# Performance work log

Measured on AMD Instinct MI355X. Metric: run time of the kernel, lower is better.

The kernel has to match this reference:

```python
import jax, jax.numpy as jnp
import numpy as np

T_SCHEDULE = 999.0
LOG_2PI = float(np.log(2.0 * np.pi))


def setup_inputs() -> dict:
    key = jax.random.key(0)
    k1, k2, k3 = jax.random.split(key, 3)
    xt = jax.random.normal(k1, (128, 3, 32, 32), dtype=jnp.float32)
    # integer-style diffusion timesteps in [0, 900); divided by t_schedule=999 inside
    t = jax.random.uniform(k2, (128,), dtype=jnp.float32) * 900.0
    gt_images = jax.random.normal(k3, (20000, 3, 32, 32), dtype=jnp.float32)
    return {"xt": xt, "t": t, "gt_images": gt_images}


def reference(xt, t, gt_images):
    # AnalyticFlow.forward_fast
    B = xt.shape[0]
    N = gt_images.shape[0]
    x = jax.lax.stop_gradient(xt.reshape(B, -1))  # original detaches x
    gt = gt_images.reshape(N, -1)                 # [N, D]
    D = x.shape[-1]
    tt = t / T_SCHEDULE                           # [B]
    sig = 1.0 - tt                                # [B]
    # log N(term_2; 0, I) summed over D, where term_2 = (x - t*gt)/(1-t).
    # ||x - t*gt||^2 = ||x||^2 - 2 t x.gt + t^2 ||gt||^2  (avoids B*N*D tensor)
    x2 = jnp.sum(x * x, axis=-1)                  # [B]
    g2 = jnp.sum(gt * gt, axis=-1)                # [N]
    xg = x @ gt.T                                 # [B, N] GEMM
    sq = x2[:, None] - 2.0 * tt[:, None] * xg + (tt * tt)[:, None] * g2[None, :]
    log_p = -0.5 * sq / (sig * sig)[:, None] - 0.5 * D * LOG_2PI  # [B, N]
    log_p = log_p - jnp.max(log_p)                # global-max shift as in original
    eta = jax.nn.softmax(log_p, axis=1)           # [B, N], rows sum to 1
    # drift = mean_n (N*eta_n) * (gt_n - x)/(1-t) = (eta @ gt - x)/(1-t)
    drift = (eta @ gt - x) / sig[:, None]         # [B, D]
    return drift.reshape(xt.shape)
```

## Files before the change

kernel.cpp:

```cpp
#include <hip/hip_runtime.h>
#include <hip/hip_bf16.h>
#include <stdint.h>

#define B_SZ   128
#define D_SZ   3072
#define N_SZ   20000
#define NPAD   20480
#define BN     (B_SZ * NPAD)
#define BD     (B_SZ * D_SZ)
#define KC_S   4
#define KC_D   20

typedef __attribute__((ext_vector_type(8))) short          short8;
typedef __attribute__((ext_vector_type(4))) float          f32x4;
typedef __attribute__((ext_vector_type(4))) unsigned short u16x4;
typedef __attribute__((ext_vector_type(2))) unsigned int   uint2v;

__device__ __forceinline__ unsigned short f2bf(float f) {
    unsigned u = __float_as_uint(f);
    u += 0x7FFFu + ((u >> 16) & 1u);
    return (unsigned short)(u >> 16);
}
__device__ __forceinline__ float bf2f(unsigned short h) {
    return __uint_as_float(((unsigned)h) << 16);
}
__device__ __forceinline__ unsigned fkey_enc(float f) {
    unsigned b = __float_as_uint(f);
    return (b & 0x80000000u) ? ~b : (b | 0x80000000u);
}
__device__ __forceinline__ float fkey_dec(unsigned u) {
    return __uint_as_float((u & 0x80000000u) ? (u ^ 0x80000000u) : ~u);
}

__device__ __forceinline__ void gl_lds16(const void* g, void* l) {
    __builtin_amdgcn_global_load_lds(
        (const __attribute__((address_space(1))) void*)g,
        (__attribute__((address_space(3))) void*)l, 16, 0, 0);
}

__device__ __forceinline__ int swz(int r, int q) { return q ^ ((r >> 1) & 3); }

__global__ __launch_bounds__(256) void zero_small(float* __restrict__ p)
{
    p[blockIdx.x * 256 + threadIdx.x] = 0.f;
}

__global__ __launch_bounds__(256) void prep_x(const float* __restrict__ x,
                                              unsigned short* __restrict__ xhi,
                                              unsigned short* __restrict__ xlo)
{
    int i = blockIdx.x * 256 + threadIdx.x;
    float v = x[i];
    unsigned short h = f2bf(v);
    xhi[i] = h;
    xlo[i] = f2bf(v - bf2f(h));
}

__global__ __launch_bounds__(256) void scores_kernel(
        const float* __restrict__ gt,
        const unsigned short* __restrict__ xhi,
        const unsigned short* __restrict__ xlo,
        float* __restrict__ XG_part,
        float* __restrict__ G2,
        unsigned short* __restrict__ Gh)
{
    __shared__ __align__(16) unsigned short Xhi_t[128 * 32];
    __shared__ __align__(16) unsigned short Xlo_t[128 * 32];
    __shared__ __align__(16) unsigned short Ghi_t[64 * 32];
    __shared__ __align__(16) unsigned short Glo_t[64 * 32];

    const int tid   = threadIdx.x;
    const int kc    = blockIdx.x & 3;
    const int nt    = blockIdx.x >> 2;
    const int nbase = nt * 64;
    const int kcb   = kc * 768;

    const int lane = tid & 63;
    const int wave = tid >> 6;
    const int mh = wave & 1;
    const int nh = wave >> 1;
    const int lm = lane & 15;
    const int qd = lane >> 4;

    const int gn = tid >> 2;
    const int gq = tid & 3;
    const int ng0 = nbase + gn;
    int grow = ng0 > N_SZ - 1 ? N_SZ - 1 : ng0;
    const float* gp0 = gt + (size_t)grow * D_SZ + kcb + gq * 8;
    unsigned short* ghp0 = Gh + (size_t)ng0 * D_SZ + kcb + gq * 8;
    const int gwr = gn * 32 + swz(gn, gq) * 8;

    int xsrc[2], xdst[2];
    #pragma unroll
    for (int i = 0; i < 2; i++) {
        int o = (i * 256 + tid) * 16;
        int r = o >> 6;
        int j = (o >> 4) & 3;
        xdst[i] = o;
        xsrc[i] = r * D_SZ + kcb + swz(r, j) * 8;
    }

    float g2acc = 0.0f;

    f32x4 acc[4][2];
    #pragma unroll
    for (int i = 0; i < 4; i++)
        #pragma unroll
        for (int j = 0; j < 2; j++)
            acc[i][j] = (f32x4){0.f, 0.f, 0.f, 0.f};

    for (int k0 = 0; k0 < 768; k0 += 32) {
        #pragma unroll
        for (int i = 0; i < 2; i++) {
            gl_lds16(xhi + xsrc[i] + k0, (char*)Xhi_t + xdst[i]);
            gl_lds16(xlo + xsrc[i] + k0, (char*)Xlo_t + xdst[i]);
        }
        f32x4 v0 = *(const f32x4*)(gp0 + k0);
        f32x4 v1 = *(const f32x4*)(gp0 + k0 + 4);
        short8 h8, l8;
        #pragma unroll
        for (int j = 0; j < 4; j++) {
            float a = v0[j], b = v1[j];
            unsigned short ha = f2bf(a), hb = f2bf(b);
            h8[j]     = (short)ha;  h8[j + 4] = (short)hb;
            l8[j]     = (short)f2bf(a - bf2f(ha));
            l8[j + 4] = (short)f2bf(b - bf2f(hb));
            g2acc += a * a + b * b;
        }
        *(short8*)&Ghi_t[gwr] = h8;
        *(short8*)&Glo_t[gwr] = l8;
        if (ng0 < N_SZ) *(short8*)(ghp0 + k0) = h8;

        __syncthreads();

        short8 bhi[2], blo[2];
        #pragma unroll
        for (int ni = 0; ni < 2; ni++) {
            int r = nh * 32 + ni * 16 + lm;
            int sl = r * 32 + swz(r, qd) * 8;
            bhi[ni] = *(short8*)&Ghi_t[sl];
            blo[ni] = *(short8*)&Glo_t[sl];
        }
        #pragma unroll
        for (int mi = 0; mi < 4; mi++) {
            int r = mh * 64 + mi * 16 + lm;
            int sl = r * 32 + swz(r, qd) * 8;
            short8 ahi = *(short8*)&Xhi_t[sl];
            short8 alo = *(short8*)&Xlo_t[sl];
            #pragma unroll
            for (int ni = 0; ni < 2; ni++) {
                acc[mi][ni] = __builtin_amdgcn_mfma_f32_16x16x32_bf16(ahi, bhi[ni], acc[mi][ni], 0, 0, 0);
                acc[mi][ni] = __builtin_amdgcn_mfma_f32_16x16x32_bf16(ahi, blo[ni], acc[mi][ni], 0, 0, 0);
                acc[mi][ni] = __builtin_amdgcn_mfma_f32_16x16x32_bf16(alo, bhi[ni], acc[mi][ni], 0, 0, 0);
            }
        }
        __syncthreads();
    }

    g2acc += __shfl_xor(g2acc, 1);
    g2acc += __shfl_xor(g2acc, 2);
    if (gq == 0 && ng0 < N_SZ) atomicAdd(&G2[ng0], g2acc);

    float* XGp = XG_part + (size_t)kc * BN;
    #pragma unroll
    for (int mi = 0; mi < 4; mi++) {
        #pragma unroll
        for (int ni = 0; ni < 2; ni++) {
            int ncol = nh * 32 + ni * 16 + lm;
            int ng = nbase + ncol;
            if (ng < N_SZ) {
                #pragma unroll
                for (int i = 0; i < 4; i++) {
                    int m = mh * 64 + mi * 16 + qd * 4 + i;
                    XGp[(size_t)m * NPAD + ng] = acc[mi][ni][i];
                }
            }
        }
    }
}

__global__ __launch_bounds__(256) void sum4max(
        const float* __restrict__ XG_part, const float* __restrict__ G2,
        const float* __restrict__ tarr, float* __restrict__ XG,
        unsigned* __restrict__ Mkey)
{
    const int tid = threadIdx.x;
    const int b = blockIdx.x / 20;
    const int i = (blockIdx.x * 256 + tid) * 4;
    __shared__ float wred[4];

    f32x4 s = (f32x4){0.f, 0.f, 0.f, 0.f};
    #pragma unroll
    for (int kc = 0; kc < KC_S; kc++)
        s += *(const f32x4*)(XG_part + (size_t)kc * BN + i);
    *(f32x4*)(XG + i) = s;

    float tt  = tarr[b] / 999.0f;
    float sig = 1.0f - tt;
    float inv = 1.0f / (sig * sig);
    float c1 = tt * inv, c2 = 0.5f * tt * tt * inv;
    int n = i - b * NPAD;

    float mx = -3.402823466e+38f;
    #pragma unroll
    for (int j = 0; j < 4; j++)
        if (n + j < N_SZ) mx = fmaxf(mx, c1 * s[j] - c2 * G2[n + j]);
    #pragma unroll
    for (int o = 32; o > 0; o >>= 1) mx = fmaxf(mx, __shfl_xor(mx, o));
    if ((tid & 63) == 0) wred[tid >> 6] = mx;
    __syncthreads();
    if (tid == 0) {
        mx = fmaxf(fmaxf(wred[0], wred[1]), fmaxf(wred[2], wred[3]));
        atomicMax(&Mkey[b], fkey_enc(mx));
    }
}

__global__ __launch_bounds__(256) void expk(
        const float* __restrict__ XG, const float* __restrict__ G2,
        const float* __restrict__ tarr, const unsigned* __restrict__ Mkey,
        unsigned short* __restrict__ P, float* __restrict__ L)
{
    const int b  = blockIdx.x >> 3;
    const int ch = blockIdx.x & 7;
    const int tid = threadIdx.x;
    float tt  = tarr[b] / 999.0f;
    float sig = 1.0f - tt;
    float inv = 1.0f / (sig * sig);
    float c1 = tt * inv, c2 = 0.5f * tt * tt * inv;
    float m = fkey_dec(Mkey[b]);
    const float* xg = XG + (size_t)b * NPAD;
    unsigned short* prow = P + (size_t)b * NPAD;
    __shared__ float wred[4];

    float sum = 0.f;
    int n0 = ch * 2560;
    for (int n = n0 + tid; n < n0 + 2560; n += 256) {
        float p = 0.f;
        if (n < N_SZ) { p = expf(c1 * xg[n] - c2 * G2[n] - m); sum += p; }
        prow[n] = f2bf(p);
    }
    #pragma unroll
    for (int o = 32; o > 0; o >>= 1) sum += __shfl_xor(sum, o);
    if ((tid & 63) == 0) wred[tid >> 6] = sum;
    __syncthreads();
    if (tid == 0) atomicAdd(&L[b], wred[0] + wred[1] + wred[2] + wred[3]);
}

__global__ __launch_bounds__(256) void drift_kernel(
        const unsigned short* __restrict__ Gh,
        const unsigned short* __restrict__ P,
        float* __restrict__ Dacc_part)
{
    __shared__ __align__(16) unsigned short Pt[128 * 32];
    __shared__ __align__(16) unsigned short Gt[128 * 40];

    const int tid = threadIdx.x;
    const int nt = blockIdx.x % 24;
    const int kc = blockIdx.x / 24;
    const int dbase = nt * 128;

    const int lane = tid & 63;
    const int wave = tid >> 6;
    const int mh = wave & 1;
    const int dh = wave >> 1;
    const int lm = lane & 15;
    const int qd = lane >> 4;

    const int dg = tid & 31;
    const int kq = tid >> 5;

    int psrc[2], pdst[2];
    #pragma unroll
    for (int i = 0; i < 2; i++) {
        int o = (i * 256 + tid) * 16;
        int r = o >> 6;
        int j = (o >> 4) & 3;
        pdst[i] = o;
        psrc[i] = r * NPAD + kc * 1024 + swz(r, j) * 8;
    }

    f32x4 acc[4][4];
    #pragma unroll
    for (int i = 0; i < 4; i++)
        #pragma unroll
        for (int j = 0; j < 4; j++)
            acc[i][j] = (f32x4){0.f, 0.f, 0.f, 0.f};

    for (int s = 0; s < 32; s++) {
        int kb = kc * 1024 + s * 32;
        #pragma unroll
        for (int i = 0; i < 2; i++)
            gl_lds16(P + psrc[i] + s * 32, (char*)Pt + pdst[i]);
        u16x4 row[4];
        #pragma unroll
        for (int i = 0; i < 4; i++) {
            int kg = kb + kq * 4 + i;
            if (kg > N_SZ - 1) kg = N_SZ - 1;
            row[i] = *(const u16x4*)(Gh + (size_t)kg * D_SZ + dbase + dg * 4);
        }
        #pragma unroll
        for (int j = 0; j < 4; j++) {
            unsigned u01 = (unsigned)row[0][j] | ((unsigned)row[1][j] << 16);
            unsigned u23 = (unsigned)row[2][j] | ((unsigned)row[3][j] << 16);
            uint2v pk = (uint2v){u01, u23};
            __builtin_memcpy((char*)Gt + (size_t)(dg * 4 + j) * 80 + kq * 8, &pk, 8);
        }
        __syncthreads();

        short8 af[4], bf8[4];
        #pragma unroll
        for (int mi = 0; mi < 4; mi++) {
            int r = mh * 64 + mi * 16 + lm;
            af[mi] = *(short8*)&Pt[r * 32 + swz(r, qd) * 8];
        }
        #pragma unroll
        for (int ni = 0; ni < 4; ni++)
            bf8[ni] = *(short8*)((char*)Gt + (size_t)(dh * 64 + ni * 16 + lm) * 80 + qd * 16);
        #pragma unroll
        for (int mi = 0; mi < 4; mi++)
            #pragma unroll
            for (int ni = 0; ni < 4; ni++)
                acc[mi][ni] = __builtin_amdgcn_mfma_f32_16x16x32_bf16(af[mi], bf8[ni], acc[mi][ni], 0, 0, 0);
        __syncthreads();
    }

    float* Dp = Dacc_part + (size_t)kc * BD;
    #pragma unroll
    for (int mi = 0; mi < 4; mi++)
        #pragma unroll
        for (int ni = 0; ni < 4; ni++) {
            int d = dbase + dh * 64 + ni * 16 + lm;
            #pragma unroll
            for (int i = 0; i < 4; i++) {
                int m = mh * 64 + mi * 16 + qd * 4 + i;
                Dp[(size_t)m * D_SZ + d] = acc[mi][ni][i];
            }
        }
}

__global__ __launch_bounds__(256) void epilogue_kernel(
        const float* __restrict__ Dacc_part, const float* __restrict__ L,
        const float* __restrict__ x, const float* __restrict__ tarr,
        float* __restrict__ out)
{
    int i = (blockIdx.x * 256 + threadIdx.x) * 4;
    int b = i / D_SZ;
    f32x4 s = (f32x4){0.f, 0.f, 0.f, 0.f};
    #pragma unroll
    for (int kc = 0; kc < KC_D; kc++)
        s += *(const f32x4*)(Dacc_part + (size_t)kc * BD + i);
    float tt = tarr[b] / 999.0f;
    float sig = 1.0f - tt;
    float invL = 1.0f / L[b];
    f32x4 xv = *(const f32x4*)(x + i);
    f32x4 o;
    #pragma unroll
    for (int j = 0; j < 4; j++) o[j] = (s[j] * invL - xv[j]) / sig;
    *(f32x4*)(out + i) = o;
}

extern "C" void kernel_launch(void* const* d_in, const int* in_sizes, int n_in,
                              void* d_out, int out_size, void* d_ws, size_t ws_size,
                              hipStream_t stream)
{
    const float* xt = (const float*)d_in[0];
    const float* t  = (const float*)d_in[1];
    const float* gt = (const float*)d_in[2];
    float* out = (float*)d_out;

    char* ws = (char*)d_ws;
    float*          XG_part  = (float*)(ws + 0);
    float*          XG       = (float*)(ws + 41943040);
    float*          Dacc_part= (float*)(ws + 52428800);
    float*          G2       = (float*)(ws + 83886080);
    unsigned*       Mkey     = (unsigned*)(ws + 83968000);
    float*          L        = (float*)(ws + 83968512);
    unsigned short* Xhi      = (unsigned short*)(ws + 83969024);
    unsigned short* Xlo      = (unsigned short*)(ws + 84755456);
    unsigned short* P        = (unsigned short*)(ws + 85541888);
    unsigned short* Gh       = (unsigned short*)(ws + 90784768);

    zero_small    <<<   81, 256, 0, stream>>>(G2);
    prep_x        <<< 1536, 256, 0, stream>>>(xt, Xhi, Xlo);
    scores_kernel <<< 1252, 256, 0, stream>>>(gt, Xhi, Xlo, XG_part, G2, Gh);
    sum4max       <<< 2560, 256, 0, stream>>>(XG_part, G2, t, XG, Mkey);
    expk          <<< 1024, 256, 0, stream>>>(XG, G2, t, Mkey, P, L);
    drift_kernel  <<<  480, 256, 0, stream>>>(Gh, P, Dacc_part);
    epilogue_kernel<<< 384, 256, 0, stream>>>(Dacc_part, L, xt, t, out);
}
```

Before: 498.3 us.

## Double-buffer LDS in scores and drift GEMMs and double drift K-split

Both GEMM kernels now use two LDS buffers. The next K-tile's global loads are issued before the MFMAs on the current tile, and the LDS stores come after them, so there is one barrier per step instead of two. The drift kernel's K-split goes from 20 to 40 chunks (960 blocks of 512 each), which raises occupancy and parallelism. The cost is twice the LDS per block, a doubled partial-sum buffer (the workspace layout shifts) and more reduction work in the epilogue.

```diff
diff --git a/kernel.cpp b/kernel.cpp
--- a/kernel.cpp
+++ b/kernel.cpp
@@ -9,7 +9,7 @@
 #define BN     (B_SZ * NPAD)
 #define BD     (B_SZ * D_SZ)
 #define KC_S   4
-#define KC_D   20
+#define KC_D   40
 
 typedef __attribute__((ext_vector_type(8))) short          short8;
 typedef __attribute__((ext_vector_type(4))) float          f32x4;
@@ -64,10 +64,10 @@
         float* __restrict__ G2,
         unsigned short* __restrict__ Gh)
 {
-    __shared__ __align__(16) unsigned short Xhi_t[128 * 32];
-    __shared__ __align__(16) unsigned short Xlo_t[128 * 32];
-    __shared__ __align__(16) unsigned short Ghi_t[64 * 32];
-    __shared__ __align__(16) unsigned short Glo_t[64 * 32];
+    __shared__ __align__(16) unsigned short Xhi_t[2][128 * 32];
+    __shared__ __align__(16) unsigned short Xlo_t[2][128 * 32];
+    __shared__ __align__(16) unsigned short Ghi_t[2][64 * 32];
+    __shared__ __align__(16) unsigned short Glo_t[2][64 * 32];
 
     const int tid   = threadIdx.x;
     const int kc    = blockIdx.x & 3;
@@ -109,50 +109,73 @@
         for (int j = 0; j < 2; j++)
             acc[i][j] = (f32x4){0.f, 0.f, 0.f, 0.f};
 
-    for (int k0 = 0; k0 < 768; k0 += 32) {
-        #pragma unroll
-        for (int i = 0; i < 2; i++) {
-            gl_lds16(xhi + xsrc[i] + k0, (char*)Xhi_t + xdst[i]);
-            gl_lds16(xlo + xsrc[i] + k0, (char*)Xlo_t + xdst[i]);
-        }
-        f32x4 v0 = *(const f32x4*)(gp0 + k0);
-        f32x4 v1 = *(const f32x4*)(gp0 + k0 + 4);
-        short8 h8, l8;
-        #pragma unroll
-        for (int j = 0; j < 4; j++) {
-            float a = v0[j], b = v1[j];
-            unsigned short ha = f2bf(a), hb = f2bf(b);
-            h8[j]     = (short)ha;  h8[j + 4] = (short)hb;
-            l8[j]     = (short)f2bf(a - bf2f(ha));
-            l8[j + 4] = (short)f2bf(b - bf2f(hb));
-            g2acc += a * a + b * b;
-        }
-        *(short8*)&Ghi_t[gwr] = h8;
-        *(short8*)&Glo_t[gwr] = l8;
-        if (ng0 < N_SZ) *(short8*)(ghp0 + k0) = h8;
-
-        __syncthreads();
-
+    #pragma unroll
+    for (int i = 0; i < 2; i++) {
+        gl_lds16(xhi + xsrc[i], (char*)Xhi_t[0] + xdst[i]);
+        gl_lds16(xlo + xsrc[i], (char*)Xlo_t[0] + xdst[i]);
+    }
+    f32x4 v0 = *(const f32x4*)(gp0);
+    f32x4 v1 = *(const f32x4*)(gp0 + 4);
+    short8 h8k, l8k;
+    #pragma unroll
+    for (int j = 0; j < 4; j++) {
+        float a = v0[j], b = v1[j];
+        unsigned short ha = f2bf(a), hb = f2bf(b);
+        h8k[j]     = (short)ha;  h8k[j + 4] = (short)hb;
+        l8k[j]     = (short)f2bf(a - bf2f(ha));
+        l8k[j + 4] = (short)f2bf(b - bf2f(hb));
+        g2acc += a * a + b * b;
+    }
+    *(short8*)&Ghi_t[0][gwr] = h8k;
+    *(short8*)&Glo_t[0][gwr] = l8k;
+    __syncthreads();
+
+    #pragma unroll 2
+    for (int t = 0; t < 24; t++) {
+        const int buf = t & 1, nxt = buf ^ 1;
+        if (ng0 < N_SZ) *(short8*)(ghp0 + t * 32) = h8k;
+        if (t < 23) {
+            #pragma unroll
+            for (int i = 0; i < 2; i++) {
+                gl_lds16(xhi + xsrc[i] + t * 32 + 32, (char*)Xhi_t[nxt] + xdst[i]);
+                gl_lds16(xlo + xsrc[i] + t * 32 + 32, (char*)Xlo_t[nxt] + xdst[i]);
+            }
+            v0 = *(const f32x4*)(gp0 + t * 32 + 32);
+            v1 = *(const f32x4*)(gp0 + t * 32 + 36);
+        }
         short8 bhi[2], blo[2];
         #pragma unroll
         for (int ni = 0; ni < 2; ni++) {
             int r = nh * 32 + ni * 16 + lm;
             int sl = r * 32 + swz(r, qd) * 8;
-            bhi[ni] = *(short8*)&Ghi_t[sl];
-            blo[ni] = *(short8*)&Glo_t[sl];
+            bhi[ni] = *(short8*)&Ghi_t[buf][sl];
+            blo[ni] = *(short8*)&Glo_t[buf][sl];
         }
         #pragma unroll
         for (int mi = 0; mi < 4; mi++) {
             int r = mh * 64 + mi * 16 + lm;
             int sl = r * 32 + swz(r, qd) * 8;
-            short8 ahi = *(short8*)&Xhi_t[sl];
-            short8 alo = *(short8*)&Xlo_t[sl];
+            short8 ahi = *(short8*)&Xhi_t[buf][sl];
+            short8 alo = *(short8*)&Xlo_t[buf][sl];
             #pragma unroll
             for (int ni = 0; ni < 2; ni++) {
                 acc[mi][ni] = __builtin_amdgcn_mfma_f32_16x16x32_bf16(ahi, bhi[ni], acc[mi][ni], 0, 0, 0);
                 acc[mi][ni] = __builtin_amdgcn_mfma_f32_16x16x32_bf16(ahi, blo[ni], acc[mi][ni], 0, 0, 0);
                 acc[mi][ni] = __builtin_amdgcn_mfma_f32_16x16x32_bf16(alo, bhi[ni], acc[mi][ni], 0, 0, 0);
             }
+        }
+        if (t < 23) {
+            #pragma unroll
+            for (int j = 0; j < 4; j++) {
+                float a = v0[j], b = v1[j];
+                unsigned short ha = f2bf(a), hb = f2bf(b);
+                h8k[j]     = (short)ha;  h8k[j + 4] = (short)hb;
+                l8k[j]     = (short)f2bf(a - bf2f(ha));
+                l8k[j + 4] = (short)f2bf(b - bf2f(hb));
+                g2acc += a * a + b * b;
+            }
+            *(short8*)&Ghi_t[nxt][gwr] = h8k;
+            *(short8*)&Glo_t[nxt][gwr] = l8k;
         }
         __syncthreads();
     }
@@ -251,13 +274,14 @@
         const unsigned short* __restrict__ P,
         float* __restrict__ Dacc_part)
 {
-    __shared__ __align__(16) unsigned short Pt[128 * 32];
-    __shared__ __align__(16) unsigned short Gt[128 * 40];
+    __shared__ __align__(16) unsigned short Pt[2][128 * 32];
+    __shared__ __align__(16) unsigned short Gt[2][128 * 40];
 
     const int tid = threadIdx.x;
     const int nt = blockIdx.x % 24;
     const int kc = blockIdx.x / 24;
     const int dbase = nt * 128;
+    const int kcb = kc * 512;
 
     const int lane = tid & 63;
     const int wave = tid >> 6;
@@ -276,7 +300,7 @@
         int r = o >> 6;
         int j = (o >> 4) & 3;
         pdst[i] = o;
-        psrc[i] = r * NPAD + kc * 1024 + swz(r, j) * 8;
+        psrc[i] = r * NPAD + kcb + swz(r, j) * 8;
     }
 
     f32x4 acc[4][4];
@@ -286,41 +310,64 @@
         for (int j = 0; j < 4; j++)
             acc[i][j] = (f32x4){0.f, 0.f, 0.f, 0.f};
 
-    for (int s = 0; s < 32; s++) {
-        int kb = kc * 1024 + s * 32;
-        #pragma unroll
-        for (int i = 0; i < 2; i++)
-            gl_lds16(P + psrc[i] + s * 32, (char*)Pt + pdst[i]);
-        u16x4 row[4];
-        #pragma unroll
-        for (int i = 0; i < 4; i++) {
-            int kg = kb + kq * 4 + i;
-            if (kg > N_SZ - 1) kg = N_SZ - 1;
-            row[i] = *(const u16x4*)(Gh + (size_t)kg * D_SZ + dbase + dg * 4);
-        }
-        #pragma unroll
-        for (int j = 0; j < 4; j++) {
-            unsigned u01 = (unsigned)row[0][j] | ((unsigned)row[1][j] << 16);
-            unsigned u23 = (unsigned)row[2][j] | ((unsigned)row[3][j] << 16);
-            uint2v pk = (uint2v){u01, u23};
-            __builtin_memcpy((char*)Gt + (size_t)(dg * 4 + j) * 80 + kq * 8, &pk, 8);
-        }
-        __syncthreads();
-
+    const unsigned short* gbase = Gh + dbase + dg * 4;
+    u16x4 row[4];
+
+    #pragma unroll
+    for (int i = 0; i < 2; i++)
+        gl_lds16(P + psrc[i], (char*)Pt[0] + pdst[i]);
+    #pragma unroll
+    for (int i = 0; i < 4; i++) {
+        int kg = kcb + kq * 4 + i;
+        if (kg > N_SZ - 1) kg = N_SZ - 1;
+        row[i] = *(const u16x4*)(gbase + (size_t)kg * D_SZ);
+    }
+    #pragma unroll
+    for (int j = 0; j < 4; j++) {
+        unsigned u01 = (unsigned)row[0][j] | ((unsigned)row[1][j] << 16);
+        unsigned u23 = (unsigned)row[2][j] | ((unsigned)row[3][j] << 16);
+        uint2v pk = (uint2v){u01, u23};
+        __builtin_memcpy((char*)Gt[0] + (size_t)(dg * 4 + j) * 80 + kq * 8, &pk, 8);
+    }
+    __syncthreads();
+
+    #pragma unroll 2
+    for (int s = 0; s < 16; s++) {
+        const int buf = s & 1, nxt = buf ^ 1;
+        if (s < 15) {
+            #pragma unroll
+            for (int i = 0; i < 2; i++)
+                gl_lds16(P + psrc[i] + (s + 1) * 32, (char*)Pt[nxt] + pdst[i]);
+            #pragma unroll
+            for (int i = 0; i < 4; i++) {
+                int kg = kcb + (s + 1) * 32 + kq * 4 + i;
+                if (kg > N_SZ - 1) kg = N_SZ - 1;
+                row[i] = *(const u16x4*)(gbase + (size_t)kg * D_SZ);
+            }
+        }
         short8 af[4], bf8[4];
         #pragma unroll
         for (int mi = 0; mi < 4; mi++) {
             int r = mh * 64 + mi * 16 + lm;
-            af[mi] = *(short8*)&Pt[r * 32 + swz(r, qd) * 8];
+            af[mi] = *(short8*)&Pt[buf][r * 32 + swz(r, qd) * 8];
         }
         #pragma unroll
         for (int ni = 0; ni < 4; ni++)
-            bf8[ni] = *(short8*)((char*)Gt + (size_t)(dh * 64 + ni * 16 + lm) * 80 + qd * 16);
+            bf8[ni] = *(short8*)((char*)Gt[buf] + (size_t)(dh * 64 + ni * 16 + lm) * 80 + qd * 16);
         #pragma unroll
         for (int mi = 0; mi < 4; mi++)
             #pragma unroll
             for (int ni = 0; ni < 4; ni++)
                 acc[mi][ni] = __builtin_amdgcn_mfma_f32_16x16x32_bf16(af[mi], bf8[ni], acc[mi][ni], 0, 0, 0);
+        if (s < 15) {
+            #pragma unroll
+            for (int j = 0; j < 4; j++) {
+                unsigned u01 = (unsigned)row[0][j] | ((unsigned)row[1][j] << 16);
+                unsigned u23 = (unsigned)row[2][j] | ((unsigned)row[3][j] << 16);
+                uint2v pk = (uint2v){u01, u23};
+                __builtin_memcpy((char*)Gt[nxt] + (size_t)(dg * 4 + j) * 80 + kq * 8, &pk, 8);
+            }
+        }
         __syncthreads();
     }
 
@@ -372,19 +419,19 @@
     float*          XG_part  = (float*)(ws + 0);
     float*          XG       = (float*)(ws + 41943040);
     float*          Dacc_part= (float*)(ws + 52428800);
-    float*          G2       = (float*)(ws + 83886080);
-    unsigned*       Mkey     = (unsigned*)(ws + 83968000);
-    float*          L        = (float*)(ws + 83968512);
-    unsigned short* Xhi      = (unsigned short*)(ws + 83969024);
-    unsigned short* Xlo      = (unsigned short*)(ws + 84755456);
-    unsigned short* P        = (unsigned short*)(ws + 85541888);
-    unsigned short* Gh       = (unsigned short*)(ws + 90784768);
+    float*          G2       = (float*)(ws + 115343360);
+    unsigned*       Mkey     = (unsigned*)(ws + 115425280);
+    float*          L        = (float*)(ws + 115425792);
+    unsigned short* Xhi      = (unsigned short*)(ws + 115426304);
+    unsigned short* Xlo      = (unsigned short*)(ws + 116212736);
+    unsigned short* P        = (unsigned short*)(ws + 116999168);
+    unsigned short* Gh       = (unsigned short*)(ws + 122242048);
 
     zero_small    <<<   81, 256, 0, stream>>>(G2);
     prep_x        <<< 1536, 256, 0, stream>>>(xt, Xhi, Xlo);
     scores_kernel <<< 1252, 256, 0, stream>>>(gt, Xhi, Xlo, XG_part, G2, Gh);
     sum4max       <<< 2560, 256, 0, stream>>>(XG_part, G2, t, XG, Mkey);
     expk          <<< 1024, 256, 0, stream>>>(XG, G2, t, Mkey, P, L);
-    drift_kernel  <<<  480, 256, 0, stream>>>(Gh, P, Dacc_part);
+    drift_kernel  <<<  960, 256, 0, stream>>>(Gh, P, Dacc_part);
     epilogue_kernel<<< 384, 256, 0, stream>>>(Dacc_part, L, xt, t, out);
 }
```

Result: no change. 495.3 us (-0.6%).

## Precompute bf16 hi/lo and transposed gt, triple-buffer async GEMM pipelines

Applied to the files above, without the earlier changes.

Adds a prep_g kernel that splits gt into bf16 hi/lo planes, computes the row norms, and writes a transposed hi copy. This lets scores_kernel and drift_kernel stream operands directly into LDS with async loads. Both GEMMs now use a three-stage LDS ring with explicit waitcnt and barriers in place of per-step syncthreads. The drift split-K count is doubled to raise the block count. The cost is an extra full pass over gt and roughly 300MB more workspace writes and reads, traded for removing in-loop conversion and the scattered transposes.

```diff
diff --git a/kernel.cpp b/kernel.cpp
--- a/kernel.cpp
+++ b/kernel.cpp
@@ -9,12 +9,10 @@
 #define BN     (B_SZ * NPAD)
 #define BD     (B_SZ * D_SZ)
 #define KC_S   4
-#define KC_D   20
+#define KC_D   40
 
 typedef __attribute__((ext_vector_type(8))) short          short8;
 typedef __attribute__((ext_vector_type(4))) float          f32x4;
-typedef __attribute__((ext_vector_type(4))) unsigned short u16x4;
-typedef __attribute__((ext_vector_type(2))) unsigned int   uint2v;
 
 __device__ __forceinline__ unsigned short f2bf(float f) {
     unsigned u = __float_as_uint(f);
@@ -56,18 +54,78 @@
     xlo[i] = f2bf(v - bf2f(h));
 }
 
+__global__ __launch_bounds__(256) void prep_g(
+        const float* __restrict__ gt,
+        unsigned short* __restrict__ Ghi,
+        unsigned short* __restrict__ Glo,
+        unsigned short* __restrict__ GhT,
+        float* __restrict__ G2)
+{
+    __shared__ unsigned short Lh[64][72];
+    const int tid = threadIdx.x;
+    const int dt  = blockIdx.x % 48;
+    const int ntl = blockIdx.x / 48;
+    const int n0 = ntl * 64, d0 = dt * 64;
+    const int r = tid >> 2, c4 = tid & 3;
+    const int n = n0 + r;
+
+    float v[16];
+    if (n < N_SZ) {
+        const float* gp = gt + (size_t)n * D_SZ + d0 + c4 * 16;
+        #pragma unroll
+        for (int i = 0; i < 4; i++) {
+            f32x4 x = *(const f32x4*)(gp + i * 4);
+            v[4*i+0] = x[0]; v[4*i+1] = x[1]; v[4*i+2] = x[2]; v[4*i+3] = x[3];
+        }
+    } else {
+        #pragma unroll
+        for (int j = 0; j < 16; j++) v[j] = 0.f;
+    }
+
+    short8 h0, h1, l0, l1;
+    float g2 = 0.f;
+    #pragma unroll
+    for (int j = 0; j < 16; j++) {
+        unsigned short h = f2bf(v[j]);
+        unsigned short l = f2bf(v[j] - bf2f(h));
+        if (j < 8) { h0[j] = (short)h; l0[j] = (short)l; }
+        else       { h1[j-8] = (short)h; l1[j-8] = (short)l; }
+        g2 += v[j] * v[j];
+        Lh[r][c4 * 16 + j] = h;
+    }
+    size_t go = (size_t)n * D_SZ + d0 + c4 * 16;
+    *(short8*)(Ghi + go)     = h0;  *(short8*)(Ghi + go + 8) = h1;
+    *(short8*)(Glo + go)     = l0;  *(short8*)(Glo + go + 8) = l1;
+
+    g2 += __shfl_xor(g2, 1);
+    g2 += __shfl_xor(g2, 2);
+    if (c4 == 0 && n < N_SZ) atomicAdd(&G2[n], g2);
+
+    __syncthreads();
+
+    const int od = tid >> 2, oc4 = tid & 3;
+    short8 t0, t1;
+    #pragma unroll
+    for (int j = 0; j < 8; j++) {
+        t0[j] = (short)Lh[oc4 * 16 + j][od];
+        t1[j] = (short)Lh[oc4 * 16 + 8 + j][od];
+    }
+    size_t to = (size_t)(d0 + od) * NPAD + n0 + oc4 * 16;
+    *(short8*)(GhT + to)     = t0;
+    *(short8*)(GhT + to + 8) = t1;
+}
+
 __global__ __launch_bounds__(256) void scores_kernel(
-        const float* __restrict__ gt,
+        const unsigned short* __restrict__ Ghi_g,
+        const unsigned short* __restrict__ Glo_g,
         const unsigned short* __restrict__ xhi,
         const unsigned short* __restrict__ xlo,
-        float* __restrict__ XG_part,
-        float* __restrict__ G2,
-        unsigned short* __restrict__ Gh)
-{
-    __shared__ __align__(16) unsigned short Xhi_t[128 * 32];
-    __shared__ __align__(16) unsigned short Xlo_t[128 * 32];
-    __shared__ __align__(16) unsigned short Ghi_t[64 * 32];
-    __shared__ __align__(16) unsigned short Glo_t[64 * 32];
+        float* __restrict__ XG_part)
+{
+    __shared__ __align__(16) unsigned short Xhi_t[3][128 * 32];
+    __shared__ __align__(16) unsigned short Xlo_t[3][128 * 32];
+    __shared__ __align__(16) unsigned short Ghi_t[3][64 * 32];
+    __shared__ __align__(16) unsigned short Glo_t[3][64 * 32];
 
     const int tid   = threadIdx.x;
     const int kc    = blockIdx.x & 3;
@@ -82,14 +140,6 @@
     const int lm = lane & 15;
     const int qd = lane >> 4;
 
-    const int gn = tid >> 2;
-    const int gq = tid & 3;
-    const int ng0 = nbase + gn;
-    int grow = ng0 > N_SZ - 1 ? N_SZ - 1 : ng0;
-    const float* gp0 = gt + (size_t)grow * D_SZ + kcb + gq * 8;
-    unsigned short* ghp0 = Gh + (size_t)ng0 * D_SZ + kcb + gq * 8;
-    const int gwr = gn * 32 + swz(gn, gq) * 8;
-
     int xsrc[2], xdst[2];
     #pragma unroll
     for (int i = 0; i < 2; i++) {
@@ -99,8 +149,9 @@
         xdst[i] = o;
         xsrc[i] = r * D_SZ + kcb + swz(r, j) * 8;
     }
-
-    float g2acc = 0.0f;
+    const int gr = tid >> 2, gs = tid & 3;
+    const int gsrc = (nbase + gr) * D_SZ + kcb + swz(gr, gs) * 8;
+    const int gdst = tid * 16;
 
     f32x4 acc[4][2];
     #pragma unroll
@@ -109,44 +160,43 @@
         for (int j = 0; j < 2; j++)
             acc[i][j] = (f32x4){0.f, 0.f, 0.f, 0.f};
 
-    for (int k0 = 0; k0 < 768; k0 += 32) {
-        #pragma unroll
-        for (int i = 0; i < 2; i++) {
-            gl_lds16(xhi + xsrc[i] + k0, (char*)Xhi_t + xdst[i]);
-            gl_lds16(xlo + xsrc[i] + k0, (char*)Xlo_t + xdst[i]);
-        }
-        f32x4 v0 = *(const f32x4*)(gp0 + k0);
-        f32x4 v1 = *(const f32x4*)(gp0 + k0 + 4);
-        short8 h8, l8;
-        #pragma unroll
-        for (int j = 0; j < 4; j++) {
-            float a = v0[j], b = v1[j];
-            unsigned short ha = f2bf(a), hb = f2bf(b);
-            h8[j]     = (short)ha;  h8[j + 4] = (short)hb;
-            l8[j]     = (short)f2bf(a - bf2f(ha));
-            l8[j + 4] = (short)f2bf(b - bf2f(hb));
-            g2acc += a * a + b * b;
-        }
-        *(short8*)&Ghi_t[gwr] = h8;
-        *(short8*)&Glo_t[gwr] = l8;
-        if (ng0 < N_SZ) *(short8*)(ghp0 + k0) = h8;
-
-        __syncthreads();
+#define STAGE_S(kk, bb) do {                                              \
+        int k0_ = (kk) * 32;                                              \
+        gl_lds16(xhi   + xsrc[0] + k0_, (char*)Xhi_t[bb] + xdst[0]);      \
+        gl_lds16(xhi   + xsrc[1] + k0_, (char*)Xhi_t[bb] + xdst[1]);      \
+        gl_lds16(xlo   + xsrc[0] + k0_, (char*)Xlo_t[bb] + xdst[0]);      \
+        gl_lds16(xlo   + xsrc[1] + k0_, (char*)Xlo_t[bb] + xdst[1]);      \
+        gl_lds16(Ghi_g + gsrc + k0_,    (char*)Ghi_t[bb] + gdst);         \
+        gl_lds16(Glo_g + gsrc + k0_,    (char*)Glo_t[bb] + gdst);         \
+    } while (0)
+
+    STAGE_S(0, 0);
+    STAGE_S(1, 1);
+
+    for (int t = 0; t < 24; t++) {
+        if (t < 23) asm volatile("s_waitcnt vmcnt(6) lgkmcnt(0)" ::: "memory");
+        else        asm volatile("s_waitcnt vmcnt(0) lgkmcnt(0)" ::: "memory");
+        __builtin_amdgcn_sched_barrier(0);
+        __builtin_amdgcn_s_barrier();
+        __builtin_amdgcn_sched_barrier(0);
+
+        const int bc = t % 3;
+        if (t < 22) { STAGE_S(t + 2, (t + 2) % 3); }
 
         short8 bhi[2], blo[2];
         #pragma unroll
         for (int ni = 0; ni < 2; ni++) {
             int r = nh * 32 + ni * 16 + lm;
             int sl = r * 32 + swz(r, qd) * 8;
-            bhi[ni] = *(short8*)&Ghi_t[sl];
-            blo[ni] = *(short8*)&Glo_t[sl];
+            bhi[ni] = *(short8*)&Ghi_t[bc][sl];
+            blo[ni] = *(short8*)&Glo_t[bc][sl];
         }
         #pragma unroll
         for (int mi = 0; mi < 4; mi++) {
             int r = mh * 64 + mi * 16 + lm;
             int sl = r * 32 + swz(r, qd) * 8;
-            short8 ahi = *(short8*)&Xhi_t[sl];
-            short8 alo = *(short8*)&Xlo_t[sl];
+            short8 ahi = *(short8*)&Xhi_t[bc][sl];
+            short8 alo = *(short8*)&Xlo_t[bc][sl];
             #pragma unroll
             for (int ni = 0; ni < 2; ni++) {
                 acc[mi][ni] = __builtin_amdgcn_mfma_f32_16x16x32_bf16(ahi, bhi[ni], acc[mi][ni], 0, 0, 0);
@@ -154,12 +204,8 @@
                 acc[mi][ni] = __builtin_amdgcn_mfma_f32_16x16x32_bf16(alo, bhi[ni], acc[mi][ni], 0, 0, 0);
             }
         }
-        __syncthreads();
-    }
-
-    g2acc += __shfl_xor(g2acc, 1);
-    g2acc += __shfl_xor(g2acc, 2);
-    if (gq == 0 && ng0 < N_SZ) atomicAdd(&G2[ng0], g2acc);
+    }
+#undef STAGE_S
 
     float* XGp = XG_part + (size_t)kc * BN;
     #pragma unroll
@@ -247,17 +293,18 @@
 }
 
 __global__ __launch_bounds__(256) void drift_kernel(
-        const unsigned short* __restrict__ Gh,
+        const unsigned short* __restrict__ GhT,
         const unsigned short* __restrict__ P,
         float* __restrict__ Dacc_part)
 {
-    __shared__ __align__(16) unsigned short Pt[128 * 32];
-    __shared__ __align__(16) unsigned short Gt[128 * 40];
+    __shared__ __align__(16) unsigned short Pt[3][128 * 32];
+    __shared__ __align__(16) unsigned short Gt[3][128 * 32];
 
     const int tid = threadIdx.x;
     const int nt = blockIdx.x % 24;
     const int kc = blockIdx.x / 24;
     const int dbase = nt * 128;
+    const int kcb = kc * 512;
 
     const int lane = tid & 63;
     const int wave = tid >> 6;
@@ -266,17 +313,15 @@
     const int lm = lane & 15;
     const int qd = lane >> 4;
 
-    const int dg = tid & 31;
-    const int kq = tid >> 5;
-
-    int psrc[2], pdst[2];
+    int psrc[2], gsrc[2], dst[2];
     #pragma unroll
     for (int i = 0; i < 2; i++) {
         int o = (i * 256 + tid) * 16;
         int r = o >> 6;
         int j = (o >> 4) & 3;
-        pdst[i] = o;
-        psrc[i] = r * NPAD + kc * 1024 + swz(r, j) * 8;
+        dst[i] = o;
+        psrc[i] = r * NPAD + kcb + swz(r, j) * 8;
+        gsrc[i] = (dbase + r) * NPAD + kcb + swz(r, j) * 8;
     }
 
     f32x4 acc[4][4];
@@ -286,43 +331,45 @@
         for (int j = 0; j < 4; j++)
             acc[i][j] = (f32x4){0.f, 0.f, 0.f, 0.f};
 
-    for (int s = 0; s < 32; s++) {
-        int kb = kc * 1024 + s * 32;
-        #pragma unroll
-        for (int i = 0; i < 2; i++)
-            gl_lds16(P + psrc[i] + s * 32, (char*)Pt + pdst[i]);
-        u16x4 row[4];
-        #pragma unroll
-        for (int i = 0; i < 4; i++) {
-            int kg = kb + kq * 4 + i;
-            if (kg > N_SZ - 1) kg = N_SZ - 1;
-            row[i] = *(const u16x4*)(Gh + (size_t)kg * D_SZ + dbase + dg * 4);
-        }
-        #pragma unroll
-        for (int j = 0; j < 4; j++) {
-            unsigned u01 = (unsigned)row[0][j] | ((unsigned)row[1][j] << 16);
-            unsigned u23 = (unsigned)row[2][j] | ((unsigned)row[3][j] << 16);
-            uint2v pk = (uint2v){u01, u23};
-            __builtin_memcpy((char*)Gt + (size_t)(dg * 4 + j) * 80 + kq * 8, &pk, 8);
-        }
-        __syncthreads();
+#define STAGE_D(ss, bb) do {                                              \
+        int k0_ = (ss) * 32;                                              \
+        gl_lds16(P   + psrc[0] + k0_, (char*)Pt[bb] + dst[0]);            \
+        gl_lds16(P   + psrc[1] + k0_, (char*)Pt[bb] + dst[1]);            \
+        gl_lds16(GhT + gsrc[0] + k0_, (char*)Gt[bb] + dst[0]);            \
+        gl_lds16(GhT + gsrc[1] + k0_, (char*)Gt[bb] + dst[1]);            \
+    } while (0)
+
+    STAGE_D(0, 0);
+    STAGE_D(1, 1);
+
+    for (int s = 0; s < 16; s++) {
+        if (s < 15) asm volatile("s_waitcnt vmcnt(4) lgkmcnt(0)" ::: "memory");
+        else        asm volatile("s_waitcnt vmcnt(0) lgkmcnt(0)" ::: "memory");
+        __builtin_amdgcn_sched_barrier(0);
+        __builtin_amdgcn_s_barrier();
+        __builtin_amdgcn_sched_barrier(0);
+
+        const int bc = s % 3;
+        if (s < 14) { STAGE_D(s + 2, (s + 2) % 3); }
 
         short8 af[4], bf8[4];
         #pragma unroll
         for (int mi = 0; mi < 4; mi++) {
             int r = mh * 64 + mi * 16 + lm;
-            af[mi] = *(short8*)&Pt[r * 32 + swz(r, qd) * 8];
-        }
-        #pragma unroll
-        for (int ni = 0; ni < 4; ni++)
-            bf8[ni] = *(short8*)((char*)Gt + (size_t)(dh * 64 + ni * 16 + lm) * 80 + qd * 16);
+            af[mi] = *(short8*)&Pt[bc][r * 32 + swz(r, qd) * 8];
+        }
+        #pragma unroll
+        for (int ni = 0; ni < 4; ni++) {
+            int r = dh * 64 + ni * 16 + lm;
+            bf8[ni] = *(short8*)&Gt[bc][r * 32 + swz(r, qd) * 8];
+        }
         #pragma unroll
         for (int mi = 0; mi < 4; mi++)
             #pragma unroll
             for (int ni = 0; ni < 4; ni++)
                 acc[mi][ni] = __builtin_amdgcn_mfma_f32_16x16x32_bf16(af[mi], bf8[ni], acc[mi][ni], 0, 0, 0);
-        __syncthreads();
-    }
+    }
+#undef STAGE_D
 
     float* Dp = Dacc_part + (size_t)kc * BD;
     #pragma unroll
@@ -372,19 +419,22 @@
     float*          XG_part  = (float*)(ws + 0);
     float*          XG       = (float*)(ws + 41943040);
     float*          Dacc_part= (float*)(ws + 52428800);
-    float*          G2       = (float*)(ws + 83886080);
-    unsigned*       Mkey     = (unsigned*)(ws + 83968000);
-    float*          L        = (float*)(ws + 83968512);
-    unsigned short* Xhi      = (unsigned short*)(ws + 83969024);
-    unsigned short* Xlo      = (unsigned short*)(ws + 84755456);
-    unsigned short* P        = (unsigned short*)(ws + 85541888);
-    unsigned short* Gh       = (unsigned short*)(ws + 90784768);
-
-    zero_small    <<<   81, 256, 0, stream>>>(G2);
-    prep_x        <<< 1536, 256, 0, stream>>>(xt, Xhi, Xlo);
-    scores_kernel <<< 1252, 256, 0, stream>>>(gt, Xhi, Xlo, XG_part, G2, Gh);
-    sum4max       <<< 2560, 256, 0, stream>>>(XG_part, G2, t, XG, Mkey);
-    expk          <<< 1024, 256, 0, stream>>>(XG, G2, t, Mkey, P, L);
-    drift_kernel  <<<  480, 256, 0, stream>>>(Gh, P, Dacc_part);
-    epilogue_kernel<<< 384, 256, 0, stream>>>(Dacc_part, L, xt, t, out);
-}
+    float*          G2       = (float*)(ws + 115343360);
+    unsigned*       Mkey     = (unsigned*)(ws + 115425280);
+    float*          L        = (float*)(ws + 115425792);
+    unsigned short* Xhi      = (unsigned short*)(ws + 115426304);
+    unsigned short* Xlo      = (unsigned short*)(ws + 116212736);
+    unsigned short* P        = (unsigned short*)(ws + 116999168);
+    unsigned short* Ghi      = (unsigned short*)(ws + 122242048);
+    unsigned short* Glo      = (unsigned short*)(ws + 248071168);
+    unsigned short* GhT      = (unsigned short*)(ws + 373900288);
+
+    zero_small    <<<    81, 256, 0, stream>>>(G2);
+    prep_x        <<<  1536, 256, 0, stream>>>(xt, Xhi, Xlo);
+    prep_g        <<< 15360, 256, 0, stream>>>(gt, Ghi, Glo, GhT, G2);
+    scores_kernel <<<  1252, 256, 0, stream>>>(Ghi, Glo, Xhi, Xlo, XG_part);
+    sum4max       <<<  2560, 256, 0, stream>>>(XG_part, G2, t, XG, Mkey);
+    expk          <<<  1024, 256, 0, stream>>>(XG, G2, t, Mkey, P, L);
+    drift_kernel  <<<   960, 256, 0, stream>>>(GhT, P, Dacc_part);
+    epilogue_kernel<<<  384, 256, 0, stream>>>(Dacc_part, L, xt, t, out);
+}
```

Result: slower. 616.5 us (+23.7%).

## Pre-tile gt into swizzled bf16 layouts and double-buffer both GEMMs

Applied to the files above, without the earlier changes.

Adds a prep_gt kernel that converts gt once into hi/lo bf16 tiles pre-swizzled for the scores GEMM and pre-transposed for the drift GEMM, and computes G2 there. Scores and drift kernels now stage tiles with direct global-to-LDS loads into double buffers, prefetching the next k-slice while computing the current one. X and P are also written pre-tiled, and drift's K split doubles to 40 chunks for more blocks. The cost is an extra pass over gt, much larger workspace writes (GS with hi and lo, plus GD), and more Dacc partials for the epilogue to reduce.

```diff
diff --git a/kernel.cpp b/kernel.cpp
--- a/kernel.cpp
+++ b/kernel.cpp
@@ -9,12 +9,12 @@
 #define BN     (B_SZ * NPAD)
 #define BD     (B_SZ * D_SZ)
 #define KC_S   4
-#define KC_D   20
+#define KC_D   40
+#define NT_S   313
+#define KS_N   96
 
 typedef __attribute__((ext_vector_type(8))) short          short8;
 typedef __attribute__((ext_vector_type(4))) float          f32x4;
-typedef __attribute__((ext_vector_type(4))) unsigned short u16x4;
-typedef __attribute__((ext_vector_type(2))) unsigned int   uint2v;
 
 __device__ __forceinline__ unsigned short f2bf(float f) {
     unsigned u = __float_as_uint(f);
@@ -46,34 +46,100 @@
 }
 
 __global__ __launch_bounds__(256) void prep_x(const float* __restrict__ x,
-                                              unsigned short* __restrict__ xhi,
-                                              unsigned short* __restrict__ xlo)
+                                              unsigned short* __restrict__ X_t)
 {
     int i = blockIdx.x * 256 + threadIdx.x;
+    int b = i / D_SZ;
+    int d = i - b * D_SZ;
+    int ks = d >> 5, c = d & 31;
     float v = x[i];
     unsigned short h = f2bf(v);
-    xhi[i] = h;
-    xlo[i] = f2bf(v - bf2f(h));
+    unsigned short l = f2bf(v - bf2f(h));
+    size_t p = (size_t)ks * 8192 + b * 32 + swz(b, c >> 3) * 8 + (c & 7);
+    X_t[p]        = h;
+    X_t[p + 4096] = l;
+}
+
+__global__ __launch_bounds__(256) void prep_gt(
+        const float* __restrict__ gt,
+        unsigned short* __restrict__ GS,
+        unsigned short* __restrict__ GD,
+        float* __restrict__ G2)
+{
+    __shared__ unsigned short Lh[64][136];
+    const int tid  = threadIdx.x;
+    const int nblk = blockIdx.x / 6;
+    const int dgrp = blockIdx.x % 6;
+    const int r  = tid >> 2, c4 = tid & 3;
+    const int n  = nblk * 64 + r;
+    const bool nv = (n < N_SZ);
+    const int ts = tid >> 7, dr = tid & 127;
+    float g2 = 0.f;
+
+    for (int cc = 0; cc < 4; cc++) {
+        const int dc = dgrp * 4 + cc;
+        const int d0 = dc * 128;
+        float v[32];
+        if (nv) {
+            const float* gp = gt + (size_t)n * D_SZ + d0 + c4 * 32;
+            #pragma unroll
+            for (int i = 0; i < 8; i++) {
+                f32x4 xv = *(const f32x4*)(gp + i * 4);
+                v[4*i+0]=xv[0]; v[4*i+1]=xv[1]; v[4*i+2]=xv[2]; v[4*i+3]=xv[3];
+            }
+        } else {
+            #pragma unroll
+            for (int j = 0; j < 32; j++) v[j] = 0.f;
+        }
+        __attribute__((aligned(16))) unsigned short h[32], l[32];
+        #pragma unroll
+        for (int j = 0; j < 32; j++) {
+            h[j] = f2bf(v[j]);
+            l[j] = f2bf(v[j] - bf2f(h[j]));
+            g2 += v[j] * v[j];
+        }
+        if (nblk < NT_S) {
+            size_t base = (size_t)(nblk * KS_N + dc * 4 + c4) * 4096 + r * 32;
+            #pragma unroll
+            for (int q = 0; q < 4; q++) {
+                *(short8*)(GS + base +        swz(r, q) * 8) = *(short8*)&h[q*8];
+                *(short8*)(GS + base + 2048 + swz(r, q) * 8) = *(short8*)&l[q*8];
+            }
+        }
+        #pragma unroll
+        for (int q = 0; q < 4; q++)
+            *(short8*)&Lh[r][c4 * 32 + q * 8] = *(short8*)&h[q*8];
+        __syncthreads();
+        {
+            __attribute__((aligned(16))) unsigned short tv[32];
+            #pragma unroll
+            for (int j = 0; j < 32; j++) tv[j] = Lh[ts * 32 + j][dr];
+            size_t base = (size_t)(dc * 640 + nblk * 2 + ts) * 4096 + dr * 32;
+            #pragma unroll
+            for (int q = 0; q < 4; q++)
+                *(short8*)(GD + base + swz(dr, q) * 8) = *(short8*)&tv[q*8];
+        }
+        __syncthreads();
+    }
+    g2 += __shfl_xor(g2, 1);
+    g2 += __shfl_xor(g2, 2);
+    if (c4 == 0 && nv) atomicAdd(&G2[n], g2);
 }
 
 __global__ __launch_bounds__(256) void scores_kernel(
-        const float* __restrict__ gt,
-        const unsigned short* __restrict__ xhi,
-        const unsigned short* __restrict__ xlo,
-        float* __restrict__ XG_part,
-        float* __restrict__ G2,
-        unsigned short* __restrict__ Gh)
-{
-    __shared__ __align__(16) unsigned short Xhi_t[128 * 32];
-    __shared__ __align__(16) unsigned short Xlo_t[128 * 32];
-    __shared__ __align__(16) unsigned short Ghi_t[64 * 32];
-    __shared__ __align__(16) unsigned short Glo_t[64 * 32];
+        const unsigned short* __restrict__ GS,
+        const unsigned short* __restrict__ X_t,
+        float* __restrict__ XG_part)
+{
+    __shared__ __align__(16) unsigned short Xh[2][4096];
+    __shared__ __align__(16) unsigned short Xl[2][4096];
+    __shared__ __align__(16) unsigned short Gh[2][2048];
+    __shared__ __align__(16) unsigned short Gl[2][2048];
 
     const int tid   = threadIdx.x;
     const int kc    = blockIdx.x & 3;
     const int nt    = blockIdx.x >> 2;
     const int nbase = nt * 64;
-    const int kcb   = kc * 768;
 
     const int lane = tid & 63;
     const int wave = tid >> 6;
@@ -82,26 +148,6 @@
     const int lm = lane & 15;
     const int qd = lane >> 4;
 
-    const int gn = tid >> 2;
-    const int gq = tid & 3;
-    const int ng0 = nbase + gn;
-    int grow = ng0 > N_SZ - 1 ? N_SZ - 1 : ng0;
-    const float* gp0 = gt + (size_t)grow * D_SZ + kcb + gq * 8;
-    unsigned short* ghp0 = Gh + (size_t)ng0 * D_SZ + kcb + gq * 8;
-    const int gwr = gn * 32 + swz(gn, gq) * 8;
-
-    int xsrc[2], xdst[2];
-    #pragma unroll
-    for (int i = 0; i < 2; i++) {
-        int o = (i * 256 + tid) * 16;
-        int r = o >> 6;
-        int j = (o >> 4) & 3;
-        xdst[i] = o;
-        xsrc[i] = r * D_SZ + kcb + swz(r, j) * 8;
-    }
-
-    float g2acc = 0.0f;
-
     f32x4 acc[4][2];
     #pragma unroll
     for (int i = 0; i < 4; i++)
@@ -109,44 +155,38 @@
         for (int j = 0; j < 2; j++)
             acc[i][j] = (f32x4){0.f, 0.f, 0.f, 0.f};
 
-    for (int k0 = 0; k0 < 768; k0 += 32) {
-        #pragma unroll
-        for (int i = 0; i < 2; i++) {
-            gl_lds16(xhi + xsrc[i] + k0, (char*)Xhi_t + xdst[i]);
-            gl_lds16(xlo + xsrc[i] + k0, (char*)Xlo_t + xdst[i]);
-        }
-        f32x4 v0 = *(const f32x4*)(gp0 + k0);
-        f32x4 v1 = *(const f32x4*)(gp0 + k0 + 4);
-        short8 h8, l8;
-        #pragma unroll
-        for (int j = 0; j < 4; j++) {
-            float a = v0[j], b = v1[j];
-            unsigned short ha = f2bf(a), hb = f2bf(b);
-            h8[j]     = (short)ha;  h8[j + 4] = (short)hb;
-            l8[j]     = (short)f2bf(a - bf2f(ha));
-            l8[j + 4] = (short)f2bf(b - bf2f(hb));
-            g2acc += a * a + b * b;
-        }
-        *(short8*)&Ghi_t[gwr] = h8;
-        *(short8*)&Glo_t[gwr] = l8;
-        if (ng0 < N_SZ) *(short8*)(ghp0 + k0) = h8;
-
-        __syncthreads();
+#define STAGE_S(ks_, bb) do {                                               \
+        size_t xb = (size_t)(ks_) * 8192;                                   \
+        size_t gb = (size_t)(nt * KS_N + (ks_)) * 4096;                     \
+        gl_lds16(X_t + xb +        tid * 8, (char*)Xh[bb] + tid * 16);      \
+        gl_lds16(X_t + xb + 2048 + tid * 8, (char*)Xh[bb] + 4096 + tid * 16);\
+        gl_lds16(X_t + xb + 4096 + tid * 8, (char*)Xl[bb] + tid * 16);      \
+        gl_lds16(X_t + xb + 6144 + tid * 8, (char*)Xl[bb] + 4096 + tid * 16);\
+        gl_lds16(GS  + gb +        tid * 8, (char*)Gh[bb] + tid * 16);      \
+        gl_lds16(GS  + gb + 2048 + tid * 8, (char*)Gl[bb] + tid * 16);      \
+    } while (0)
+
+    STAGE_S(kc * 24, 0);
+    __syncthreads();
+
+    for (int t = 0; t < 24; t++) {
+        const int buf = t & 1;
+        if (t < 23) STAGE_S(kc * 24 + t + 1, buf ^ 1);
 
         short8 bhi[2], blo[2];
         #pragma unroll
         for (int ni = 0; ni < 2; ni++) {
             int r = nh * 32 + ni * 16 + lm;
             int sl = r * 32 + swz(r, qd) * 8;
-            bhi[ni] = *(short8*)&Ghi_t[sl];
-            blo[ni] = *(short8*)&Glo_t[sl];
+            bhi[ni] = *(short8*)&Gh[buf][sl];
+            blo[ni] = *(short8*)&Gl[buf][sl];
         }
         #pragma unroll
         for (int mi = 0; mi < 4; mi++) {
             int r = mh * 64 + mi * 16 + lm;
             int sl = r * 32 + swz(r, qd) * 8;
-            short8 ahi = *(short8*)&Xhi_t[sl];
-            short8 alo = *(short8*)&Xlo_t[sl];
+            short8 ahi = *(short8*)&Xh[buf][sl];
+            short8 alo = *(short8*)&Xl[buf][sl];
             #pragma unroll
             for (int ni = 0; ni < 2; ni++) {
                 acc[mi][ni] = __builtin_amdgcn_mfma_f32_16x16x32_bf16(ahi, bhi[ni], acc[mi][ni], 0, 0, 0);
@@ -156,10 +196,7 @@
         }
         __syncthreads();
     }
-
-    g2acc += __shfl_xor(g2acc, 1);
-    g2acc += __shfl_xor(g2acc, 2);
-    if (gq == 0 && ng0 < N_SZ) atomicAdd(&G2[ng0], g2acc);
+#undef STAGE_S
 
     float* XGp = XG_part + (size_t)kc * BN;
     #pragma unroll
@@ -218,7 +255,7 @@
 __global__ __launch_bounds__(256) void expk(
         const float* __restrict__ XG, const float* __restrict__ G2,
         const float* __restrict__ tarr, const unsigned* __restrict__ Mkey,
-        unsigned short* __restrict__ P, float* __restrict__ L)
+        unsigned short* __restrict__ P_t, float* __restrict__ L)
 {
     const int b  = blockIdx.x >> 3;
     const int ch = blockIdx.x & 7;
@@ -229,7 +266,6 @@
     float c1 = tt * inv, c2 = 0.5f * tt * tt * inv;
     float m = fkey_dec(Mkey[b]);
     const float* xg = XG + (size_t)b * NPAD;
-    unsigned short* prow = P + (size_t)b * NPAD;
     __shared__ float wred[4];
 
     float sum = 0.f;
@@ -237,7 +273,8 @@
     for (int n = n0 + tid; n < n0 + 2560; n += 256) {
         float p = 0.f;
         if (n < N_SZ) { p = expf(c1 * xg[n] - c2 * G2[n] - m); sum += p; }
-        prow[n] = f2bf(p);
+        int c = n & 31;
+        P_t[(size_t)(n >> 5) * 4096 + b * 32 + swz(b, c >> 3) * 8 + (c & 7)] = f2bf(p);
     }
     #pragma unroll
     for (int o = 32; o > 0; o >>= 1) sum += __shfl_xor(sum, o);
@@ -247,17 +284,17 @@
 }
 
 __global__ __launch_bounds__(256) void drift_kernel(
-        const unsigned short* __restrict__ Gh,
-        const unsigned short* __restrict__ P,
+        const unsigned short* __restrict__ GD,
+        const unsigned short* __restrict__ P_t,
         float* __restrict__ Dacc_part)
 {
-    __shared__ __align__(16) unsigned short Pt[128 * 32];
-    __shared__ __align__(16) unsigned short Gt[128 * 40];
+    __shared__ __align__(16) unsigned short Pt[2][4096];
+    __shared__ __align__(16) unsigned short Gt[2][4096];
 
     const int tid = threadIdx.x;
-    const int nt = blockIdx.x % 24;
+    const int dt = blockIdx.x % 24;
     const int kc = blockIdx.x / 24;
-    const int dbase = nt * 128;
+    const int dbase = dt * 128;
 
     const int lane = tid & 63;
     const int wave = tid >> 6;
@@ -266,19 +303,6 @@
     const int lm = lane & 15;
     const int qd = lane >> 4;
 
-    const int dg = tid & 31;
-    const int kq = tid >> 5;
-
-    int psrc[2], pdst[2];
-    #pragma unroll
-    for (int i = 0; i < 2; i++) {
-        int o = (i * 256 + tid) * 16;
-        int r = o >> 6;
-        int j = (o >> 4) & 3;
-        pdst[i] = o;
-        psrc[i] = r * NPAD + kc * 1024 + swz(r, j) * 8;
-    }
-
     f32x4 acc[4][4];
     #pragma unroll
     for (int i = 0; i < 4; i++)
@@ -286,36 +310,33 @@
         for (int j = 0; j < 4; j++)
             acc[i][j] = (f32x4){0.f, 0.f, 0.f, 0.f};
 
-    for (int s = 0; s < 32; s++) {
-        int kb = kc * 1024 + s * 32;
-        #pragma unroll
-        for (int i = 0; i < 2; i++)
-            gl_lds16(P + psrc[i] + s * 32, (char*)Pt + pdst[i]);
-        u16x4 row[4];
-        #pragma unroll
-        for (int i = 0; i < 4; i++) {
-            int kg = kb + kq * 4 + i;
-            if (kg > N_SZ - 1) kg = N_SZ - 1;
-            row[i] = *(const u16x4*)(Gh + (size_t)kg * D_SZ + dbase + dg * 4);
-        }
-        #pragma unroll
-        for (int j = 0; j < 4; j++) {
-            unsigned u01 = (unsigned)row[0][j] | ((unsigned)row[1][j] << 16);
-            unsigned u23 = (unsigned)row[2][j] | ((unsigned)row[3][j] << 16);
-            uint2v pk = (uint2v){u01, u23};
-            __builtin_memcpy((char*)Gt + (size_t)(dg * 4 + j) * 80 + kq * 8, &pk, 8);
-        }
-        __syncthreads();
+#define STAGE_D(ns_, bb) do {                                               \
+        size_t pb = (size_t)(ns_) * 4096;                                   \
+        size_t gb = (size_t)(dt * 640 + (ns_)) * 4096;                      \
+        gl_lds16(P_t + pb +        tid * 8, (char*)Pt[bb] + tid * 16);      \
+        gl_lds16(P_t + pb + 2048 + tid * 8, (char*)Pt[bb] + 4096 + tid * 16);\
+        gl_lds16(GD  + gb +        tid * 8, (char*)Gt[bb] + tid * 16);      \
+        gl_lds16(GD  + gb + 2048 + tid * 8, (char*)Gt[bb] + 4096 + tid * 16);\
+    } while (0)
+
+    STAGE_D(kc * 16, 0);
+    __syncthreads();
+
+    for (int s = 0; s < 16; s++) {
+        const int buf = s & 1;
+        if (s < 15) STAGE_D(kc * 16 + s + 1, buf ^ 1);
 
         short8 af[4], bf8[4];
         #pragma unroll
         for (int mi = 0; mi < 4; mi++) {
             int r = mh * 64 + mi * 16 + lm;
-            af[mi] = *(short8*)&Pt[r * 32 + swz(r, qd) * 8];
-        }
-        #pragma unroll
-        for (int ni = 0; ni < 4; ni++)
-            bf8[ni] = *(short8*)((char*)Gt + (size_t)(dh * 64 + ni * 16 + lm) * 80 + qd * 16);
+            af[mi] = *(short8*)&Pt[buf][r * 32 + swz(r, qd) * 8];
+        }
+        #pragma unroll
+        for (int ni = 0; ni < 4; ni++) {
+            int r = dh * 64 + ni * 16 + lm;
+            bf8[ni] = *(short8*)&Gt[buf][r * 32 + swz(r, qd) * 8];
+        }
         #pragma unroll
         for (int mi = 0; mi < 4; mi++)
             #pragma unroll
@@ -323,6 +344,7 @@
                 acc[mi][ni] = __builtin_amdgcn_mfma_f32_16x16x32_bf16(af[mi], bf8[ni], acc[mi][ni], 0, 0, 0);
         __syncthreads();
     }
+#undef STAGE_D
 
     float* Dp = Dacc_part + (size_t)kc * BD;
     #pragma unroll
@@ -372,19 +394,20 @@
     float*          XG_part  = (float*)(ws + 0);
     float*          XG       = (float*)(ws + 41943040);
     float*          Dacc_part= (float*)(ws + 52428800);
-    float*          G2       = (float*)(ws + 83886080);
-    unsigned*       Mkey     = (unsigned*)(ws + 83968000);
-    float*          L        = (float*)(ws + 83968512);
-    unsigned short* Xhi      = (unsigned short*)(ws + 83969024);
-    unsigned short* Xlo      = (unsigned short*)(ws + 84755456);
-    unsigned short* P        = (unsigned short*)(ws + 85541888);
-    unsigned short* Gh       = (unsigned short*)(ws + 90784768);
+    float*          G2       = (float*)(ws + 115343360);
+    unsigned*       Mkey     = (unsigned*)(ws + 115425280);
+    float*          L        = (float*)(ws + 115425792);
+    unsigned short* X_t      = (unsigned short*)(ws + 115426304);
+    unsigned short* P_t      = (unsigned short*)(ws + 116999168);
+    unsigned short* GS       = (unsigned short*)(ws + 122242048);
+    unsigned short* GD       = (unsigned short*)(ws + 368395264);
 
     zero_small    <<<   81, 256, 0, stream>>>(G2);
-    prep_x        <<< 1536, 256, 0, stream>>>(xt, Xhi, Xlo);
-    scores_kernel <<< 1252, 256, 0, stream>>>(gt, Xhi, Xlo, XG_part, G2, Gh);
+    prep_x        <<< 1536, 256, 0, stream>>>(xt, X_t);
+    prep_gt       <<< 1920, 256, 0, stream>>>(gt, GS, GD, G2);
+    scores_kernel <<< 1252, 256, 0, stream>>>(GS, X_t, XG_part);
     sum4max       <<< 2560, 256, 0, stream>>>(XG_part, G2, t, XG, Mkey);
-    expk          <<< 1024, 256, 0, stream>>>(XG, G2, t, Mkey, P, L);
-    drift_kernel  <<<  480, 256, 0, stream>>>(Gh, P, Dacc_part);
+    expk          <<< 1024, 256, 0, stream>>>(XG, G2, t, Mkey, P_t, L);
+    drift_kernel  <<<  960, 256, 0, stream>>>(GD, P_t, Dacc_part);
     epilogue_kernel<<< 384, 256, 0, stream>>>(Dacc_part, L, xt, t, out);
 }
```

Measured after the change: 620.9 us. 1.25x slower.
